# Kernel tuning notes

Hardware: AMD Instinct MI355X
Metric: run time of the kernel (lower is better)

## Reference

```python
import jax, jax.numpy as jnp
import numpy as np

R = 16
ALPHA = 32
SCALING = ALPHA / R  # 2.0


def setup_inputs() -> dict:
    key = jax.random.key(0)
    k_x, k_w, k_b, k_a, k_bm = jax.random.split(key, 5)
    d = 1024
    x = jax.random.normal(k_x, (4, 4096, d), dtype=jnp.float32)
    W = jax.random.normal(k_w, (d, d), dtype=jnp.float32) * 0.02
    b = jax.random.normal(k_b, (d,), dtype=jnp.float32) * 0.02
    A = jax.random.normal(k_a, (R, d), dtype=jnp.float32) * 0.02
    B = jax.random.normal(k_bm, (d, R), dtype=jnp.float32) * 0.02
    return {"x": x, "W": W, "b": b, "A": A, "B": B}


def reference(x, W, b, A, B):
    # base linear: x @ W^T + b   (W: [out, in])
    base = jnp.einsum("bsd,od->bso", x, W) + b
    # low-rank update: (x @ A^T) @ B^T, scaled (dropout p=0 -> identity)
    u = jnp.einsum("bsd,rd->bsr", x, A)   # [B, S, r]
    update = jnp.einsum("bsr,or->bso", u, B)
    return base + SCALING * update
```

## Files before the change

### kernel.cpp

```cpp
#include <hip/hip_runtime.h>


typedef __bf16 bf16x8 __attribute__((ext_vector_type(8)));
typedef float f32x4 __attribute__((ext_vector_type(4)));
typedef unsigned short ushort8 __attribute__((ext_vector_type(8)));

__device__ __forceinline__ unsigned short f2bf(float f) {
    __bf16 h = (__bf16)f;
    union { __bf16 b; unsigned short u; } v; v.b = h; return v.u;
}
__device__ __forceinline__ ushort8 cvt8(f32x4 a, f32x4 b) {
    ushort8 o;
#pragma unroll
    for (int i = 0; i < 4; ++i) { o[i] = f2bf(a[i]); o[i + 4] = f2bf(b[i]); }
    return o;
}
__device__ __forceinline__ void gld16(const unsigned short* g, unsigned short* l) {
    __builtin_amdgcn_global_load_lds(
        (const __attribute__((address_space(1))) unsigned int*)g,
        (__attribute__((address_space(3))) unsigned int*)l, 16, 0, 0);
}

#define FENCE() asm volatile("" ::: "memory")
#define BARRIER() do { FENCE(); __builtin_amdgcn_s_barrier(); FENCE(); } while (0)

__global__ __launch_bounds__(256) void prep(
    const float* __restrict__ X, const float* __restrict__ W,
    const float* __restrict__ A, const float* __restrict__ B,
    unsigned short* __restrict__ xbf, unsigned short* __restrict__ Weff)
{
    const int b = blockIdx.x;
    if (b < 512) {
        const int idx = b * 256 + threadIdx.x;
        const int o  = idx >> 7;
        const int kc = (idx & 127) << 3;
        float br[16];
#pragma unroll
        for (int r = 0; r < 16; ++r) br[r] = 2.0f * B[o * 16 + r];
        float acc[8];
        const float* wrow = W + (size_t)o * 1024 + kc;
#pragma unroll
        for (int j = 0; j < 8; ++j) acc[j] = wrow[j];
#pragma unroll
        for (int r = 0; r < 16; ++r) {
            const float* arow = A + r * 1024 + kc;
#pragma unroll
            for (int j = 0; j < 8; ++j) acc[j] += br[r] * arow[j];
        }
        ushort8 o8;
#pragma unroll
        for (int j = 0; j < 8; ++j) o8[j] = f2bf(acc[j]);
        *(ushort8*)(Weff + (size_t)o * 1024 + kc) = o8;
    } else {
        const size_t i = ((size_t)(b - 512) * 256 + threadIdx.x) * 8;
        f32x4 a = *(const f32x4*)(X + i);
        f32x4 c = *(const f32x4*)(X + i + 4);
        *(ushort8*)(xbf + i) = cvt8(a, c);
    }
}

template<int MH, int NH>
__device__ __forceinline__ void qmfma(f32x4 (&acc)[8][4],
                                      const bf16x8 (&fa)[8][2],
                                      const bf16x8 (&fb)[4][2]) {
#pragma unroll
    for (int m2 = 0; m2 < 4; ++m2)
#pragma unroll
        for (int n2 = 0; n2 < 2; ++n2)
#pragma unroll
            for (int ks = 0; ks < 2; ++ks)
                acc[MH * 4 + m2][NH * 2 + n2] = __builtin_amdgcn_mfma_f32_16x16x32_bf16(
                    fa[MH * 4 + m2][ks], fb[NH * 2 + n2][ks],
                    acc[MH * 4 + m2][NH * 2 + n2], 0, 0, 0);
}

#define PHASE_MFMA(MH, NH)                                          \
    do { BARRIER();                                                 \
         asm volatile("s_waitcnt lgkmcnt(0)" ::: "memory");         \
         __builtin_amdgcn_sched_barrier(0);            \
         __builtin_amdgcn_s_setprio(1);                             \
         qmfma<MH, NH>(acc, fa, fb);                                \
         __builtin_amdgcn_s_setprio(0);                             \
         BARRIER(); } while (0)

__global__ __launch_bounds__(512, 2) void gemm256(
    const unsigned short* __restrict__ Xb,
    const unsigned short* __restrict__ Wt,
    const float* __restrict__ bias,
    float* __restrict__ out)
{
    extern __shared__ __align__(16) unsigned short lds[];

    const int t    = threadIdx.x;
    const int lane = t & 63;
    const int w    = t >> 6;
    const int wr   = w >> 2;
    const int wc   = w & 3;
    const int r16  = lane & 15;
    const int quad = lane >> 4;

    const int nwg = gridDim.x;
    int swz = blockIdx.x;
    if ((nwg & 7) == 0) swz = (swz & 7) * (nwg >> 3) + (swz >> 3);
    const int bm = (swz >> 2) * 256;
    const int bn = (swz & 3) * 256;

    const int c0 = w * 128 + lane, c1 = c0 + 64;
    const int r0 = c0 >> 3,        r1 = c1 >> 3;
    const int s0c = (c0 & 7) ^ (r0 & 7);
    const int s1c = (c1 & 7) ^ (r1 & 7);
    const unsigned short* pA0 = Xb + (size_t)(bm + r0) * 1024 + s0c * 8;
    const unsigned short* pA1 = Xb + (size_t)(bm + r1) * 1024 + s1c * 8;
    const unsigned short* pB0 = Wt + (size_t)(bn + r0) * 1024 + s0c * 8;
    const unsigned short* pB1 = Wt + (size_t)(bn + r1) * 1024 + s1c * 8;
    const int lc0 = c0 * 8, lc1 = c1 * 8;

    const int ck    = (quad ^ (r16 & 7)) * 8;
    const int aBase = wr * 8192 + r16 * 64 + ck;
    const int bBase = 16384 + (wc >> 1) * 8192 + (wc & 1) * 4096 + r16 * 64 + ck;

    f32x4 acc[8][4];
#pragma unroll
    for (int i = 0; i < 8; ++i)
#pragma unroll
        for (int jj = 0; jj < 4; ++jj)
            acc[i][jj] = (f32x4){0.f, 0.f, 0.f, 0.f};

    gld16(pA0,               lds + lc0);            gld16(pA1,               lds + lc1);            FENCE();
    gld16(pA0 + 131072,      lds + 8192  + lc0);    gld16(pA1 + 131072,      lds + 8192  + lc1);    FENCE();
    gld16(pB0,               lds + 16384 + lc0);    gld16(pB1,               lds + 16384 + lc1);    FENCE();
    gld16(pB0 + 131072,      lds + 24576 + lc0);    gld16(pB1 + 131072,      lds + 24576 + lc1);    FENCE();
    gld16(pA0 + 64,          lds + 32768 + lc0);    gld16(pA1 + 64,          lds + 32768 + lc1);    FENCE();
    gld16(pA0 + 131072 + 64, lds + 40960 + lc0);    gld16(pA1 + 131072 + 64, lds + 40960 + lc1);    FENCE();
    gld16(pB0 + 64,          lds + 49152 + lc0);    gld16(pB1 + 64,          lds + 49152 + lc1);
    asm volatile("s_waitcnt vmcnt(6)" ::: "memory");
    BARRIER();

#pragma unroll 2
    for (int j = 0; j < 16; ++j) {
        const unsigned short* Lb = lds + (j & 1) * 32768;
        unsigned short* Sc = lds + (j & 1) * 32768;
        unsigned short* Sn = lds + ((j & 1) ^ 1) * 32768;
        const int k1 = (j + 1) * 64, k2 = (j + 2) * 64;

        bf16x8 fa[8][2], fb[4][2];

#pragma unroll
        for (int mt = 0; mt < 4; ++mt) {
            fa[mt][0] = *(const bf16x8*)(Lb + aBase + mt * 1024);
            fa[mt][1] = *(const bf16x8*)(Lb + (aBase ^ 32) + mt * 1024);
        }
#pragma unroll
        for (int nt = 0; nt < 2; ++nt) {
            fb[nt][0] = *(const bf16x8*)(Lb + bBase + nt * 1024);
            fb[nt][1] = *(const bf16x8*)(Lb + (bBase ^ 32) + nt * 1024);
        }
        if (wr == 0) {
#pragma unroll
            for (int mt = 4; mt < 8; ++mt) {
                fa[mt][0] = *(const bf16x8*)(Lb + aBase + mt * 1024);
                fa[mt][1] = *(const bf16x8*)(Lb + (aBase ^ 32) + mt * 1024);
            }
        }
        if (j < 15) { gld16(pB0 + 131072 + k1, Sn + 24576 + lc0);
                      gld16(pB1 + 131072 + k1, Sn + 24576 + lc1); }
        PHASE_MFMA(0, 0);

        if (wr == 1) {
#pragma unroll
            for (int mt = 4; mt < 8; ++mt) {
                fa[mt][0] = *(const bf16x8*)(Lb + aBase + mt * 1024);
                fa[mt][1] = *(const bf16x8*)(Lb + (aBase ^ 32) + mt * 1024);
            }
        }
#pragma unroll
        for (int nt = 2; nt < 4; ++nt) {
            fb[nt][0] = *(const bf16x8*)(Lb + bBase + nt * 1024);
            fb[nt][1] = *(const bf16x8*)(Lb + (bBase ^ 32) + nt * 1024);
        }
        if (j < 14) { gld16(pA0 + k2, Sc + lc0);
                      gld16(pA1 + k2, Sc + lc1); }
        PHASE_MFMA(0, 1);

        if (j < 14) { gld16(pA0 + 131072 + k2, Sc + 8192 + lc0);
                      gld16(pA1 + 131072 + k2, Sc + 8192 + lc1); }
        PHASE_MFMA(1, 1);

        if (j < 14) { gld16(pB0 + k2, Sc + 16384 + lc0);
                      gld16(pB1 + k2, Sc + 16384 + lc1); }
        if (j < 14)       asm volatile("s_waitcnt vmcnt(6)" ::: "memory");
        else if (j == 14) asm volatile("s_waitcnt vmcnt(0)" ::: "memory");
        PHASE_MFMA(1, 0);
    }

    const int orow0 = bm + wr * 128 + quad * 4;
    const int ocol0 = bn + wc * 64 + r16;
#pragma unroll
    for (int nt = 0; nt < 4; ++nt) {
        const float bv = bias[ocol0 + nt * 16];
#pragma unroll
        for (int mt = 0; mt < 8; ++mt) {
            float* orow = out + (size_t)(orow0 + mt * 16) * 1024 + (ocol0 + nt * 16);
#pragma unroll
            for (int i = 0; i < 4; ++i)
                orow[(size_t)i * 1024] = acc[mt][nt][i] + bv;
        }
    }
}

template <bool XF32>
__global__ __launch_bounds__(256) void gemm_bt(
    const void* __restrict__ X_, const unsigned short* __restrict__ Wt,
    const float* __restrict__ bias, float* __restrict__ out)
{
    __shared__ __align__(16) unsigned short lA[128 * 32];
    __shared__ __align__(16) unsigned short lB[128 * 32];

    const int t    = threadIdx.x;
    const int lane = t & 63;
    const int w    = t >> 6;
    const int bm   = blockIdx.x * 128;
    const int bn   = blockIdx.y * 128;
    const int wm   = (w & 1) * 64;
    const int wn   = (w >> 1) * 64;
    const int r16  = lane & 15;
    const int quad = lane >> 4;

    const int srow = t >> 2;
    const int gc   = (t & 3) ^ ((srow >> 1) & 3);
    unsigned short* lsA = lA + t * 8;
    unsigned short* lsB = lB + t * 8;
    const size_t ga0 = (size_t)(bm + srow) * 1024 + gc * 8;
    const size_t ga1 = (size_t)(bm + srow + 64) * 1024 + gc * 8;
    const unsigned short* gB0 = Wt + (size_t)(bn + srow) * 1024 + gc * 8;

    const int p    = (quad ^ ((r16 >> 1) & 3)) * 8;
    const int aoff = (wm + r16) * 32 + p;
    const int boff = (wn + r16) * 32 + p;

    const unsigned short* Xb = (const unsigned short*)X_;
    const float*          Xf = (const float*)X_;

    f32x4 acc[4][4];
#pragma unroll
    for (int i = 0; i < 4; ++i)
#pragma unroll
        for (int j = 0; j < 4; ++j) {
            f32x4 z = {0.f, 0.f, 0.f, 0.f};
            acc[i][j] = z;
        }

    for (int kt = 0; kt < 1024; kt += 32) {
        if (XF32) {
            f32x4 a0 = *(const f32x4*)(Xf + ga0 + kt);
            f32x4 a1 = *(const f32x4*)(Xf + ga0 + kt + 4);
            f32x4 a2 = *(const f32x4*)(Xf + ga1 + kt);
            f32x4 a3 = *(const f32x4*)(Xf + ga1 + kt + 4);
            *(ushort8*)lsA          = cvt8(a0, a1);
            *(ushort8*)(lsA + 2048) = cvt8(a2, a3);
        } else {
            gld16(Xb + ga0 + kt, lsA);
            gld16(Xb + ga1 + kt, lsA + 2048);
        }
        gld16(gB0 + kt,             lsB);
        gld16(gB0 + kt + 64 * 1024, lsB + 2048);
        __syncthreads();

        bf16x8 fa[4], fb[4];
#pragma unroll
        for (int mt = 0; mt < 4; ++mt) fa[mt] = *(const bf16x8*)(lA + aoff + mt * 16 * 32);
#pragma unroll
        for (int nt = 0; nt < 4; ++nt) fb[nt] = *(const bf16x8*)(lB + boff + nt * 16 * 32);

#pragma unroll
        for (int mt = 0; mt < 4; ++mt)
#pragma unroll
            for (int nt = 0; nt < 4; ++nt)
                acc[mt][nt] = __builtin_amdgcn_mfma_f32_16x16x32_bf16(
                    fa[mt], fb[nt], acc[mt][nt], 0, 0, 0);

        __syncthreads();
    }

    const int orow0 = bm + wm + quad * 4;
    const int ocol0 = bn + wn + r16;
#pragma unroll
    for (int nt = 0; nt < 4; ++nt) {
        const float bv = bias[ocol0 + nt * 16];
#pragma unroll
        for (int mt = 0; mt < 4; ++mt)
#pragma unroll
            for (int i = 0; i < 4; ++i)
                out[(size_t)(orow0 + mt * 16 + i) * 1024 + (ocol0 + nt * 16)] =
                    acc[mt][nt][i] + bv;
    }
}

extern "C" void kernel_launch(void* const* d_in, const int* in_sizes, int n_in,
                              void* d_out, int out_size, void* d_ws, size_t ws_size,
                              hipStream_t stream) {
    const float* x  = (const float*)d_in[0];
    const float* W  = (const float*)d_in[1];
    const float* b  = (const float*)d_in[2];
    const float* A  = (const float*)d_in[3];
    const float* Bm = (const float*)d_in[4];
    float* out = (float*)d_out;

    const int M = in_sizes[0] / 1024;

    const bool fast = (ws_size >= ((size_t)(M)*1024*2 + (2u << 20) + 4096)) &&
                      (M % 256 == 0);
    if (fast) {
        unsigned short* xbf  = (unsigned short*)d_ws;
        unsigned short* Weff = xbf + (size_t)M * 1024;
        hipLaunchKernelGGL(prep, dim3(512 + M / 2), dim3(256), 0, stream,
                           x, W, A, Bm, xbf, Weff);
        hipLaunchKernelGGL(gemm256, dim3((M / 256) * 4), dim3(512), 131072, stream,
                           xbf, Weff, b, out);
    } else {
        unsigned short* Weff = (unsigned short*)d_ws;
        hipLaunchKernelGGL(prep, dim3(512), dim3(256), 0, stream,
                           x, W, A, Bm, (unsigned short*)nullptr, Weff);
        hipLaunchKernelGGL((gemm_bt<true>), dim3(M / 128, 8), dim3(256), 0, stream,
                           (const void*)x, Weff, b, out);
    }
}
```

Baseline: 174.9 us.

## Interleave wave-to-tile mapping and reorder LDS fragment loads and prefetches

Changes how waves map onto the 256x256 output tile. Each wave now takes interleaved 16-row and 16-column subtiles with strides of 32 rows and 64 columns, instead of contiguous 128x64 blocks. Fragment reads from LDS are regrouped so all waves load the second half of A after the first MFMA phases, which removes the wave-divergent wr branches. The global prefetch order is shuffled and an explicit lgkmcnt wait is added. The aim is to balance LDS bank access and overlap loads with MFMA better, at the cost of more scattered output stores.

```diff
diff --git a/kernel.cpp b/kernel.cpp
--- a/kernel.cpp
+++ b/kernel.cpp
@@ -115,9 +115,9 @@
     const unsigned short* pB1 = Wt + (size_t)(bn + r1) * 1024 + s1c * 8;
     const int lc0 = c0 * 8, lc1 = c1 * 8;
 
-    const int ck    = (quad ^ (r16 & 7)) * 8;
-    const int aBase = wr * 8192 + r16 * 64 + ck;
-    const int bBase = 16384 + (wc >> 1) * 8192 + (wc & 1) * 4096 + r16 * 64 + ck;
+    const int sw  = (quad ^ (r16 & 7)) * 8;
+    const int aB  = wr * 1024 + r16 * 64 + sw;
+    const int bB  = 16384 + wc * 1024 + r16 * 64 + sw;
 
     f32x4 acc[8][4];
 #pragma unroll
@@ -127,12 +127,12 @@
             acc[i][jj] = (f32x4){0.f, 0.f, 0.f, 0.f};
 
     gld16(pA0,               lds + lc0);            gld16(pA1,               lds + lc1);            FENCE();
+    gld16(pB0,               lds + 16384 + lc0);    gld16(pB1,               lds + 16384 + lc1);    FENCE();
     gld16(pA0 + 131072,      lds + 8192  + lc0);    gld16(pA1 + 131072,      lds + 8192  + lc1);    FENCE();
-    gld16(pB0,               lds + 16384 + lc0);    gld16(pB1,               lds + 16384 + lc1);    FENCE();
     gld16(pB0 + 131072,      lds + 24576 + lc0);    gld16(pB1 + 131072,      lds + 24576 + lc1);    FENCE();
     gld16(pA0 + 64,          lds + 32768 + lc0);    gld16(pA1 + 64,          lds + 32768 + lc1);    FENCE();
-    gld16(pA0 + 131072 + 64, lds + 40960 + lc0);    gld16(pA1 + 131072 + 64, lds + 40960 + lc1);    FENCE();
-    gld16(pB0 + 64,          lds + 49152 + lc0);    gld16(pB1 + 64,          lds + 49152 + lc1);
+    gld16(pB0 + 64,          lds + 49152 + lc0);    gld16(pB1 + 64,          lds + 49152 + lc1);    FENCE();
+    gld16(pA0 + 131072 + 64, lds + 40960 + lc0);    gld16(pA1 + 131072 + 64, lds + 40960 + lc1);
     asm volatile("s_waitcnt vmcnt(6)" ::: "memory");
     BARRIER();
 
@@ -147,60 +147,52 @@
 
 #pragma unroll
         for (int mt = 0; mt < 4; ++mt) {
-            fa[mt][0] = *(const bf16x8*)(Lb + aBase + mt * 1024);
-            fa[mt][1] = *(const bf16x8*)(Lb + (aBase ^ 32) + mt * 1024);
+            fa[mt][0] = *(const bf16x8*)(Lb + aB + mt * 2048);
+            fa[mt][1] = *(const bf16x8*)(Lb + ((aB + mt * 2048) ^ 32));
         }
 #pragma unroll
         for (int nt = 0; nt < 2; ++nt) {
-            fb[nt][0] = *(const bf16x8*)(Lb + bBase + nt * 1024);
-            fb[nt][1] = *(const bf16x8*)(Lb + (bBase ^ 32) + nt * 1024);
-        }
-        if (wr == 0) {
-#pragma unroll
-            for (int mt = 4; mt < 8; ++mt) {
-                fa[mt][0] = *(const bf16x8*)(Lb + aBase + mt * 1024);
-                fa[mt][1] = *(const bf16x8*)(Lb + (aBase ^ 32) + mt * 1024);
-            }
+            fb[nt][0] = *(const bf16x8*)(Lb + bB + nt * 4096);
+            fb[nt][1] = *(const bf16x8*)(Lb + ((bB + nt * 4096) ^ 32));
         }
         if (j < 15) { gld16(pB0 + 131072 + k1, Sn + 24576 + lc0);
                       gld16(pB1 + 131072 + k1, Sn + 24576 + lc1); }
+        asm volatile("s_waitcnt lgkmcnt(8)" ::: "memory");
         PHASE_MFMA(0, 0);
 
-        if (wr == 1) {
-#pragma unroll
-            for (int mt = 4; mt < 8; ++mt) {
-                fa[mt][0] = *(const bf16x8*)(Lb + aBase + mt * 1024);
-                fa[mt][1] = *(const bf16x8*)(Lb + (aBase ^ 32) + mt * 1024);
-            }
-        }
 #pragma unroll
         for (int nt = 2; nt < 4; ++nt) {
-            fb[nt][0] = *(const bf16x8*)(Lb + bBase + nt * 1024);
-            fb[nt][1] = *(const bf16x8*)(Lb + (bBase ^ 32) + nt * 1024);
+            fb[nt][0] = *(const bf16x8*)(Lb + bB + 8192 + (nt - 2) * 4096);
+            fb[nt][1] = *(const bf16x8*)(Lb + ((bB + 8192 + (nt - 2) * 4096) ^ 32));
         }
         if (j < 14) { gld16(pA0 + k2, Sc + lc0);
                       gld16(pA1 + k2, Sc + lc1); }
         PHASE_MFMA(0, 1);
 
+#pragma unroll
+        for (int mt = 4; mt < 8; ++mt) {
+            fa[mt][0] = *(const bf16x8*)(Lb + aB + 8192 + (mt - 4) * 2048);
+            fa[mt][1] = *(const bf16x8*)(Lb + ((aB + 8192 + (mt - 4) * 2048) ^ 32));
+        }
+        if (j < 14) { gld16(pB0 + k2, Sc + 16384 + lc0);
+                      gld16(pB1 + k2, Sc + 16384 + lc1); }
+        PHASE_MFMA(1, 1);
+
         if (j < 14) { gld16(pA0 + 131072 + k2, Sc + 8192 + lc0);
                       gld16(pA1 + 131072 + k2, Sc + 8192 + lc1); }
-        PHASE_MFMA(1, 1);
-
-        if (j < 14) { gld16(pB0 + k2, Sc + 16384 + lc0);
-                      gld16(pB1 + k2, Sc + 16384 + lc1); }
         if (j < 14)       asm volatile("s_waitcnt vmcnt(6)" ::: "memory");
         else if (j == 14) asm volatile("s_waitcnt vmcnt(0)" ::: "memory");
         PHASE_MFMA(1, 0);
     }
 
-    const int orow0 = bm + wr * 128 + quad * 4;
-    const int ocol0 = bn + wc * 64 + r16;
+    const int orow0 = bm + wr * 16 + quad * 4;
+    const int ocol0 = bn + wc * 16 + r16;
 #pragma unroll
     for (int nt = 0; nt < 4; ++nt) {
-        const float bv = bias[ocol0 + nt * 16];
+        const float bv = bias[ocol0 + nt * 64];
 #pragma unroll
         for (int mt = 0; mt < 8; ++mt) {
-            float* orow = out + (size_t)(orow0 + mt * 16) * 1024 + (ocol0 + nt * 16);
+            float* orow = out + (size_t)(orow0 + mt * 32) * 1024 + (ocol0 + nt * 64);
 #pragma unroll
             for (int i = 0; i < 4; ++i)
                 orow[(size_t)i * 1024] = acc[mt][nt][i] + bv;
```

After: 151.9 us. 1.15x faster.
